# Optimization experiments

Measured on AMD Instinct MI355X. Metric: run time of the kernel, lower is better.

## Reference

```python
import jax, jax.numpy as jnp
import numpy as np

E, D, H, K, T = 16, 1024, 2048, 2, 2048


def setup_inputs() -> dict:
    key = jax.random.key(0)
    k = jax.random.split(key, 7)
    scale = 0.02
    return {
        "inp": jax.random.normal(k[0], (T, D), dtype=jnp.float32),
        "gate_idx": jax.random.randint(k[1], (T, K), 0, E, dtype=jnp.int64),
        "gate_score": jax.random.uniform(k[2], (T, K), dtype=jnp.float32),
        "w1": jax.random.normal(k[3], (E, H, D), dtype=jnp.float32) * scale,
        "b1": jnp.zeros((E, H), dtype=jnp.float32),
        "w2": jax.random.normal(k[4], (E, D, H), dtype=jnp.float32) * scale,
        "b2": jnp.zeros((E, D), dtype=jnp.float32),
    }


def reference(inp, gate_idx, gate_score, w1, b1, w2, b2):
    num_expert = w1.shape[0]
    top_k = gate_idx.shape[1]
    d_model = inp.shape[1]
    # expand each token top_k times (repeat_interleave along dim 0)
    x = jnp.repeat(inp, top_k, axis=0)           # [T*K, D]
    g = gate_idx.reshape(-1)                      # [T*K]
    o = jnp.zeros((x.shape[0], d_model), dtype=x.dtype)
    # static loop over experts; output masked by expert assignment (same math
    # as the per-expert gather/scatter in the original)
    for i in range(num_expert):
        h = jax.nn.gelu(x @ w1[i].T + b1[i])      # [T*K, H]
        y = h @ w2[i].T + b2[i]                   # [T*K, D]
        o = o + jnp.where((g == i)[:, None], y, jnp.zeros((), x.dtype))
    # combine top_k expert outputs with gate scores (bmm in the original)
    out = jnp.einsum("nk,nkd->nd", gate_score, o.reshape(-1, top_k, d_model))
    return out
```

## Files before the change

kernel.cpp:

```cpp
#include <hip/hip_runtime.h>
#include <hip/hip_bf16.h>
#include <stdint.h>


#define E_ 16
#define D_ 1024
#define H_ 2048
#define K_ 2
#define T_ 2048
#define NP_ (T_ * K_)
#define MTS_ 48

using short8 = __attribute__((ext_vector_type(8))) short;
using f32x4  = __attribute__((ext_vector_type(4))) float;

__device__ __forceinline__ unsigned short f2bf(float f) {
  union { float f; unsigned u; } x; x.f = f;
  unsigned r = x.u + 0x7fffu + ((x.u >> 16) & 1u);
  return (unsigned short)(r >> 16);
}

__device__ __forceinline__ float gelu_f(float x) {
  float u = 1.5957691216057308f * (x + 0.044715f * x * x * x);
  return x / (1.f + __expf(-u));
}

__global__ void cvt_kernel(const float* __restrict__ src,
                           unsigned short* __restrict__ dst, int n4) {
  int stride = gridDim.x * blockDim.x;
  for (int i = blockIdx.x * blockDim.x + threadIdx.x; i < n4; i += stride) {
    float4 v = reinterpret_cast<const float4*>(src)[i];
    ushort4 o = make_ushort4(f2bf(v.x), f2bf(v.y), f2bf(v.z), f2bf(v.w));
    reinterpret_cast<ushort4*>(dst)[i] = o;
  }
}

__global__ void route_kernel(const int* __restrict__ gidx,
                             int* __restrict__ rows,
                             int* __restrict__ offsets,
                             int2* __restrict__ tiles) {
  __shared__ int cnt[E_], cur[E_];
  int tid = threadIdx.x;
  if (tid < E_) cnt[tid] = 0;
  __syncthreads();
  for (int p = tid; p < NP_; p += blockDim.x) atomicAdd(&cnt[gidx[p]], 1);
  __syncthreads();
  if (tid == 0) {
    int acc = 0;
    for (int e = 0; e < E_; ++e) { offsets[e] = acc; cur[e] = acc; acc += cnt[e]; }
    offsets[E_] = acc;
    int k = 0;
    for (int e = 0; e < E_; ++e)
      for (int m = offsets[e]; m < offsets[e] + cnt[e]; m += 128)
        tiles[k++] = make_int2(e, m);
    for (; k < MTS_; ++k) tiles[k] = make_int2(-1, 0);
  }
  __syncthreads();
  for (int p = tid; p < NP_; p += blockDim.x) {
    int e = gidx[p];
    int pos = atomicAdd(&cur[e], 1);
    rows[pos] = p;
  }
}

#define GLOAD16(g, l)                                                        \
  __builtin_amdgcn_global_load_lds(                                          \
      (const __attribute__((address_space(1))) unsigned int*)(const void*)(g), \
      (__attribute__((address_space(3))) unsigned int*)(void*)(l), 16, 0, 0)

template<bool IS1>
__global__ __launch_bounds__(256, 3)
void moe_gemm(const unsigned short* __restrict__ A0,
              const float* __restrict__ W,
              const float* __restrict__ bias,
              const int* __restrict__ rows,
              const int* __restrict__ offsets,
              const int2* __restrict__ tiles,
              const float* __restrict__ score,
              unsigned short* __restrict__ Hout,
              float* __restrict__ Yout)
{
  constexpr int BM = 128, BN = 64, BK = 64;
  constexpr int KD = IS1 ? D_ : H_;
  constexpr int NN = IS1 ? H_ : D_;
  constexpr int NT = KD / BK;

  const int2 tile = tiles[blockIdx.y];
  const int e = tile.x;
  if (e < 0) return;
  const int s0   = tile.y;
  const int send = offsets[e + 1];
  const int n0   = blockIdx.x * BN;

  __shared__ unsigned short As[2][BM][BK];
  __shared__ unsigned short Bs[2][BN][BK + 8];
  __shared__ int rowsrc[BM];
  __shared__ int rowdst[BM];

  const int tid  = threadIdx.x;
  const int lane = tid & 63;
  const int wid  = tid >> 6;

  if (tid < BM) {
    int s = s0 + tid;
    bool v = s < send;
    int sc2 = v ? s : s0;
    if (IS1) {
      rowsrc[tid] = rows[sc2] >> 1;
      rowdst[tid] = v ? s : -1;
    } else {
      rowsrc[tid] = sc2;
      rowdst[tid] = v ? rows[s] : -1;
    }
  }
  __syncthreads();

  const int arow  = lane >> 3;
  const int aslot = (lane & 7) ^ arow;
  const unsigned short* gA[4];
#pragma unroll
  for (int i = 0; i < 4; ++i)
    gA[i] = A0 + (size_t)rowsrc[wid * 32 + i * 8 + arow] * KD + aslot * 8;

  const int brow = tid >> 2, bseg = tid & 3;
  const float* gB = W + (size_t)e * NN * KD + (size_t)(n0 + brow) * KD + bseg * 16;

  const int wr = wid >> 1, wc = wid & 1;
  const int fr = lane & 15, fh = lane >> 4;

  f32x4 acc[4][2] = {};
  float4 breg[4];

  auto stageA = [&](int buf, int kk) {
#pragma unroll
    for (int i = 0; i < 4; ++i)
      GLOAD16(gA[i] + kk, &As[buf][wid * 32 + i * 8][0]);
  };
  auto loadB = [&](int kk) {
#pragma unroll
    for (int j = 0; j < 4; ++j)
      breg[j] = *reinterpret_cast<const float4*>(gB + kk + j * 4);
  };
  auto writeB = [&](int buf) {
#pragma unroll
    for (int h = 0; h < 2; ++h) {
      short8 v;
#pragma unroll
      for (int q = 0; q < 4; ++q) v[q]     = (short)f2bf((&breg[2*h].x)[q]);
#pragma unroll
      for (int q = 0; q < 4; ++q) v[4 + q] = (short)f2bf((&breg[2*h+1].x)[q]);
      *reinterpret_cast<short8*>(&Bs[buf][brow][bseg * 16 + h * 8]) = v;
    }
  };
  auto compute = [&](int buf) {
    short8 af[4][2], bv[2][2];
#pragma unroll
    for (int mi = 0; mi < 4; ++mi) {
      const int row = wr * 64 + mi * 16 + fr;
#pragma unroll
      for (int ks = 0; ks < 2; ++ks) {
        const int slot = (ks * 4 + fh) ^ (fr & 7);
        af[mi][ks] = *reinterpret_cast<const short8*>(&As[buf][row][slot * 8]);
      }
    }
#pragma unroll
    for (int ni = 0; ni < 2; ++ni) {
      const int row = wc * 32 + ni * 16 + fr;
#pragma unroll
      for (int ks = 0; ks < 2; ++ks)
        bv[ni][ks] = *reinterpret_cast<const short8*>(&Bs[buf][row][ks * 32 + fh * 8]);
    }
#pragma unroll
    for (int ks = 0; ks < 2; ++ks)
#pragma unroll
      for (int mi = 0; mi < 4; ++mi)
#pragma unroll
        for (int ni = 0; ni < 2; ++ni)
          acc[mi][ni] = __builtin_amdgcn_mfma_f32_16x16x32_bf16(
              af[mi][ks], bv[ni][ks], acc[mi][ni], 0, 0, 0);
  };

  loadB(0);
  stageA(0, 0);
  writeB(0);
  __syncthreads();

  for (int t = 0; t < NT; t += 2) {
    loadB((t + 1) * BK);
    stageA(1, (t + 1) * BK);
    compute(0);
    writeB(1);
    __syncthreads();
    if (t + 2 < NT) { loadB((t + 2) * BK); stageA(0, (t + 2) * BK); }
    compute(1);
    if (t + 2 < NT) writeB(0);
    __syncthreads();
  }

  const float* biasE = bias + (size_t)e * NN + n0;
#pragma unroll
  for (int mi = 0; mi < 4; ++mi) {
#pragma unroll
    for (int j = 0; j < 4; ++j) {
      int rt  = wr * 64 + mi * 16 + fh * 4 + j;
      int dst = rowdst[rt];
      if (dst < 0) continue;
      float sc = IS1 ? 0.f : score[dst];
#pragma unroll
      for (int ni = 0; ni < 2; ++ni) {
        int col = wc * 32 + ni * 16 + fr;
        float v = acc[mi][ni][j] + biasE[col];
        if (IS1) {
          Hout[(size_t)dst * H_ + n0 + col] = f2bf(gelu_f(v));
        } else {
          Yout[(size_t)dst * D_ + n0 + col] = v * sc;
        }
      }
    }
  }
}

__global__ void combine_kernel(const float* __restrict__ y,
                               float* __restrict__ out) {
  const int DQ = D_ / 4;
  int i = blockIdx.x * blockDim.x + threadIdx.x;
  int t = i / DQ, d = i % DQ;
  const float4* y4 = reinterpret_cast<const float4*>(y);
  float4 a = y4[(size_t)(2 * t) * DQ + d];
  float4 b = y4[(size_t)(2 * t + 1) * DQ + d];
  reinterpret_cast<float4*>(out)[i] =
      make_float4(a.x + b.x, a.y + b.y, a.z + b.z, a.w + b.w);
}

extern "C" void kernel_launch(void* const* d_in, const int* in_sizes, int n_in,
                              void* d_out, int out_size, void* d_ws, size_t ws_size,
                              hipStream_t stream) {
  const float* inp    = (const float*)d_in[0];
  const int*   gidx   = (const int*)d_in[1];
  const float* gscore = (const float*)d_in[2];
  const float* w1     = (const float*)d_in[3];
  const float* b1     = (const float*)d_in[4];
  const float* w2     = (const float*)d_in[5];
  const float* b2     = (const float*)d_in[6];
  float* out = (float*)d_out;

  char* ws = (char*)d_ws;
  size_t o = 0;
  auto alloc = [&](size_t bytes) {
    void* p = ws + o;
    o = (o + bytes + 255) & ~(size_t)255;
    return p;
  };
  unsigned short* xb   = (unsigned short*)alloc((size_t)T_ * D_ * 2);
  unsigned short* hbuf = (unsigned short*)alloc((size_t)NP_ * H_ * 2);
  float*          ybuf = (float*)alloc((size_t)NP_ * D_ * 4);
  int*            rows = (int*)alloc(NP_ * 4);
  int*         offsets = (int*)alloc((E_ + 1) * 4);
  int2*          tiles = (int2*)alloc(MTS_ * 8);

  cvt_kernel<<<dim3(256), dim3(256), 0, stream>>>(inp, xb, T_ * D_ / 4);
  route_kernel<<<dim3(1), dim3(256), 0, stream>>>(gidx, rows, offsets, tiles);

  moe_gemm<true><<<dim3(H_ / 64, MTS_, 1), dim3(256), 0, stream>>>(
      xb, w1, b1, rows, offsets, tiles, gscore, hbuf, (float*)nullptr);
  moe_gemm<false><<<dim3(D_ / 64, MTS_, 1), dim3(256), 0, stream>>>(
      hbuf, w2, b2, rows, offsets, tiles, gscore, (unsigned short*)nullptr, ybuf);

  combine_kernel<<<dim3(T_ * D_ / 4 / 256), dim3(256), 0, stream>>>(ybuf, out);
}
```

Before: 171.6 us.

## Deepen GEMM prefetch with two B register sets and explicit vmcnt waits

The MoE GEMM main loop now keeps two tiles of loads in flight, using two register buffers for the fp32 weights and issuing the next A/B loads before converting and storing the current B tile. Raw s_waitcnt and s_barrier with scheduling barriers replace __syncthreads so that outstanding global loads are not fully drained at each barrier. The padded B shared-memory tile is replaced by an XOR-swizzled layout to avoid bank conflicts without padding. The cvt kernel grid is also doubled. The hand-counted vmcnt(8) waits depend on the exact number of loads the compiler emits, so a miscount could let the code read stale LDS.

```diff
diff --git a/kernel.cpp b/kernel.cpp
--- a/kernel.cpp
+++ b/kernel.cpp
@@ -23,6 +23,26 @@
 __device__ __forceinline__ float gelu_f(float x) {
   float u = 1.5957691216057308f * (x + 0.044715f * x * x * x);
   return x / (1.f + __expf(-u));
+}
+
+__device__ __forceinline__ void waitv8() {
+  asm volatile("s_waitcnt vmcnt(8)" ::: "memory");
+  __builtin_amdgcn_sched_barrier(0);
+}
+__device__ __forceinline__ void waitv0() {
+  asm volatile("s_waitcnt vmcnt(0)" ::: "memory");
+  __builtin_amdgcn_sched_barrier(0);
+}
+__device__ __forceinline__ void barrier_only() {
+  __builtin_amdgcn_sched_barrier(0);
+  __builtin_amdgcn_s_barrier();
+  __builtin_amdgcn_sched_barrier(0);
+}
+__device__ __forceinline__ void lgkm0_barrier() {
+  asm volatile("s_waitcnt lgkmcnt(0)" ::: "memory");
+  __builtin_amdgcn_sched_barrier(0);
+  __builtin_amdgcn_s_barrier();
+  __builtin_amdgcn_sched_barrier(0);
 }
 
 __global__ void cvt_kernel(const float* __restrict__ src,
@@ -93,7 +113,7 @@
   const int n0   = blockIdx.x * BN;
 
   __shared__ unsigned short As[2][BM][BK];
-  __shared__ unsigned short Bs[2][BN][BK + 8];
+  __shared__ unsigned short Bs[2][BN][BK];
   __shared__ int rowsrc[BM];
   __shared__ int rowdst[BM];
 
@@ -129,27 +149,28 @@
   const int fr = lane & 15, fh = lane >> 4;
 
   f32x4 acc[4][2] = {};
-  float4 breg[4];
-
-  auto stageA = [&](int buf, int kk) {
+  float4 breg0[4], breg1[4];
+
+  auto issueA = [&](int buf, int kk) {
 #pragma unroll
     for (int i = 0; i < 4; ++i)
       GLOAD16(gA[i] + kk, &As[buf][wid * 32 + i * 8][0]);
   };
-  auto loadB = [&](int kk) {
+  auto issueB = [&](float4* br, int kk) {
 #pragma unroll
     for (int j = 0; j < 4; ++j)
-      breg[j] = *reinterpret_cast<const float4*>(gB + kk + j * 4);
-  };
-  auto writeB = [&](int buf) {
-#pragma unroll
-    for (int h = 0; h < 2; ++h) {
+      br[j] = *reinterpret_cast<const float4*>(gB + kk + j * 4);
+  };
+  auto writeB = [&](int buf, const float4* br) {
+#pragma unroll
+    for (int j = 0; j < 2; ++j) {
       short8 v;
 #pragma unroll
-      for (int q = 0; q < 4; ++q) v[q]     = (short)f2bf((&breg[2*h].x)[q]);
-#pragma unroll
-      for (int q = 0; q < 4; ++q) v[4 + q] = (short)f2bf((&breg[2*h+1].x)[q]);
-      *reinterpret_cast<short8*>(&Bs[buf][brow][bseg * 16 + h * 8]) = v;
+      for (int q = 0; q < 4; ++q) v[q]     = (short)f2bf((&br[2*j].x)[q]);
+#pragma unroll
+      for (int q = 0; q < 4; ++q) v[4 + q] = (short)f2bf((&br[2*j+1].x)[q]);
+      int slot = (bseg * 2 + j) ^ (brow & 7);
+      *reinterpret_cast<short8*>(&Bs[buf][brow][slot * 8]) = v;
     }
   };
   auto compute = [&](int buf) {
@@ -159,7 +180,7 @@
       const int row = wr * 64 + mi * 16 + fr;
 #pragma unroll
       for (int ks = 0; ks < 2; ++ks) {
-        const int slot = (ks * 4 + fh) ^ (fr & 7);
+        const int slot = (ks * 4 + fh) ^ (row & 7);
         af[mi][ks] = *reinterpret_cast<const short8*>(&As[buf][row][slot * 8]);
       }
     }
@@ -167,8 +188,10 @@
     for (int ni = 0; ni < 2; ++ni) {
       const int row = wc * 32 + ni * 16 + fr;
 #pragma unroll
-      for (int ks = 0; ks < 2; ++ks)
-        bv[ni][ks] = *reinterpret_cast<const short8*>(&Bs[buf][row][ks * 32 + fh * 8]);
+      for (int ks = 0; ks < 2; ++ks) {
+        const int slot = (ks * 4 + fh) ^ (row & 7);
+        bv[ni][ks] = *reinterpret_cast<const short8*>(&Bs[buf][row][slot * 8]);
+      }
     }
 #pragma unroll
     for (int ks = 0; ks < 2; ++ks)
@@ -180,21 +203,31 @@
               af[mi][ks], bv[ni][ks], acc[mi][ni], 0, 0, 0);
   };
 
-  loadB(0);
-  stageA(0, 0);
-  writeB(0);
-  __syncthreads();
+  issueA(0, 0);       issueB(breg0, 0);
+  issueA(1, BK);      issueB(breg1, BK);
+  waitv8();
+  writeB(0, breg0);
+  lgkm0_barrier();
 
   for (int t = 0; t < NT; t += 2) {
-    loadB((t + 1) * BK);
-    stageA(1, (t + 1) * BK);
     compute(0);
-    writeB(1);
-    __syncthreads();
-    if (t + 2 < NT) { loadB((t + 2) * BK); stageA(0, (t + 2) * BK); }
+    barrier_only();
+    if (t + 2 < NT) {
+      issueA(0, (t + 2) * BK); issueB(breg0, (t + 2) * BK);
+      waitv8();
+    } else {
+      waitv0();
+    }
+    writeB(1, breg1);
+    lgkm0_barrier();
     compute(1);
-    if (t + 2 < NT) writeB(0);
-    __syncthreads();
+    barrier_only();
+    if (t + 2 < NT) {
+      if (t + 3 < NT) { issueA(1, (t + 3) * BK); issueB(breg1, (t + 3) * BK); waitv8(); }
+      else            { waitv0(); }
+      writeB(0, breg0);
+      lgkm0_barrier();
+    }
   }
 
   const float* biasE = bias + (size_t)e * NN + n0;
@@ -258,7 +291,7 @@
   int*         offsets = (int*)alloc((E_ + 1) * 4);
   int2*          tiles = (int2*)alloc(MTS_ * 8);
 
-  cvt_kernel<<<dim3(256), dim3(256), 0, stream>>>(inp, xb, T_ * D_ / 4);
+  cvt_kernel<<<dim3(512), dim3(256), 0, stream>>>(inp, xb, T_ * D_ / 4);
   route_kernel<<<dim3(1), dim3(256), 0, stream>>>(gidx, rows, offsets, tiles);
 
   moe_gemm<true><<<dim3(H_ / 64, MTS_, 1), dim3(256), 0, stream>>>(
```

Result: faster. 157.1 us (-8.5%).

## Replace LDS-tiled MoE GEMM with register-only flat MFMA kernel

Applied to the files above, without the earlier changes.

Rewrites both expert GEMMs so operands come straight from global memory into registers, with no LDS staging and no barriers. Weights act as the MFMA A operand (128 output features per block) and token rows as B (128 tokens per tile). Loads are double-buffered in registers across K steps of 32. This removes the LDS traffic and syncthreads overhead, at the cost of redundant global/L2 reads of activations per wave, higher register pressure and fewer blocks.

```diff
diff --git a/kernel.cpp b/kernel.cpp
--- a/kernel.cpp
+++ b/kernel.cpp
@@ -63,14 +63,9 @@
   }
 }
 
-#define GLOAD16(g, l)                                                        \
-  __builtin_amdgcn_global_load_lds(                                          \
-      (const __attribute__((address_space(1))) unsigned int*)(const void*)(g), \
-      (__attribute__((address_space(3))) unsigned int*)(void*)(l), 16, 0, 0)
-
 template<bool IS1>
-__global__ __launch_bounds__(256, 3)
-void moe_gemm(const unsigned short* __restrict__ A0,
+__global__ __launch_bounds__(256, 2)
+void moe_flat(const unsigned short* __restrict__ Bsrc,
               const float* __restrict__ W,
               const float* __restrict__ bias,
               const int* __restrict__ rows,
@@ -80,141 +75,101 @@
               unsigned short* __restrict__ Hout,
               float* __restrict__ Yout)
 {
-  constexpr int BM = 128, BN = 64, BK = 64;
   constexpr int KD = IS1 ? D_ : H_;
   constexpr int NN = IS1 ? H_ : D_;
-  constexpr int NT = KD / BK;
+  constexpr int NT = KD / 32;
 
   const int2 tile = tiles[blockIdx.y];
   const int e = tile.x;
   if (e < 0) return;
   const int s0   = tile.y;
   const int send = offsets[e + 1];
-  const int n0   = blockIdx.x * BN;
-
-  __shared__ unsigned short As[2][BM][BK];
-  __shared__ unsigned short Bs[2][BN][BK + 8];
-  __shared__ int rowsrc[BM];
-  __shared__ int rowdst[BM];
-
-  const int tid  = threadIdx.x;
-  const int lane = tid & 63;
-  const int wid  = tid >> 6;
-
-  if (tid < BM) {
-    int s = s0 + tid;
-    bool v = s < send;
-    int sc2 = v ? s : s0;
-    if (IS1) {
-      rowsrc[tid] = rows[sc2] >> 1;
-      rowdst[tid] = v ? s : -1;
-    } else {
-      rowsrc[tid] = sc2;
-      rowdst[tid] = v ? rows[s] : -1;
+
+  const int tid = threadIdx.x, lane = tid & 63, wid = tid >> 6;
+  const int fr = lane & 15, fh = lane >> 4;
+
+  const int abase = blockIdx.x * 128 + wid * 32;
+
+  const float* gA0 = W + ((size_t)e * NN + abase + fr) * KD + fh * 8;
+  const float* gA1 = gA0 + (size_t)16 * KD;
+
+  int boff[8];
+#pragma unroll
+  for (int ni = 0; ni < 8; ++ni) {
+    int slot = s0 + ni * 16 + fr;
+    int cs   = slot < send ? slot : (send - 1);
+    int br   = IS1 ? (rows[cs] >> 1) : cs;
+    boff[ni] = br * KD;
+  }
+  const unsigned short* gBb = Bsrc + fh * 8;
+
+  f32x4 acc[2][8] = {};
+  short8 b0[8], b1[8];
+  float4 a0[2][2], a1[2][2];
+
+  auto loadB = [&](short8* b, int k0) {
+#pragma unroll
+    for (int ni = 0; ni < 8; ++ni)
+      b[ni] = *reinterpret_cast<const short8*>(gBb + boff[ni] + k0);
+  };
+  auto loadA = [&](float4 (*a)[2], int k0) {
+    a[0][0] = *reinterpret_cast<const float4*>(gA0 + k0);
+    a[0][1] = *reinterpret_cast<const float4*>(gA0 + k0 + 4);
+    a[1][0] = *reinterpret_cast<const float4*>(gA1 + k0);
+    a[1][1] = *reinterpret_cast<const float4*>(gA1 + k0 + 4);
+  };
+  auto step = [&](float4 (*a)[2], short8* b) {
+#pragma unroll
+    for (int mi = 0; mi < 2; ++mi) {
+      short8 av;
+      const float* f0 = &a[mi][0].x;
+      const float* f1 = &a[mi][1].x;
+#pragma unroll
+      for (int q = 0; q < 4; ++q) {
+        av[q]     = (short)f2bf(f0[q]);
+        av[4 + q] = (short)f2bf(f1[q]);
+      }
+#pragma unroll
+      for (int ni = 0; ni < 8; ++ni)
+        acc[mi][ni] = __builtin_amdgcn_mfma_f32_16x16x32_bf16(
+            av, b[ni], acc[mi][ni], 0, 0, 0);
     }
-  }
-  __syncthreads();
-
-  const int arow  = lane >> 3;
-  const int aslot = (lane & 7) ^ arow;
-  const unsigned short* gA[4];
-#pragma unroll
-  for (int i = 0; i < 4; ++i)
-    gA[i] = A0 + (size_t)rowsrc[wid * 32 + i * 8 + arow] * KD + aslot * 8;
-
-  const int brow = tid >> 2, bseg = tid & 3;
-  const float* gB = W + (size_t)e * NN * KD + (size_t)(n0 + brow) * KD + bseg * 16;
-
-  const int wr = wid >> 1, wc = wid & 1;
-  const int fr = lane & 15, fh = lane >> 4;
-
-  f32x4 acc[4][2] = {};
-  float4 breg[4];
-
-  auto stageA = [&](int buf, int kk) {
-#pragma unroll
-    for (int i = 0; i < 4; ++i)
-      GLOAD16(gA[i] + kk, &As[buf][wid * 32 + i * 8][0]);
-  };
-  auto loadB = [&](int kk) {
-#pragma unroll
-    for (int j = 0; j < 4; ++j)
-      breg[j] = *reinterpret_cast<const float4*>(gB + kk + j * 4);
-  };
-  auto writeB = [&](int buf) {
-#pragma unroll
-    for (int h = 0; h < 2; ++h) {
-      short8 v;
-#pragma unroll
-      for (int q = 0; q < 4; ++q) v[q]     = (short)f2bf((&breg[2*h].x)[q]);
-#pragma unroll
-      for (int q = 0; q < 4; ++q) v[4 + q] = (short)f2bf((&breg[2*h+1].x)[q]);
-      *reinterpret_cast<short8*>(&Bs[buf][brow][bseg * 16 + h * 8]) = v;
-    }
-  };
-  auto compute = [&](int buf) {
-    short8 af[4][2], bv[2][2];
-#pragma unroll
-    for (int mi = 0; mi < 4; ++mi) {
-      const int row = wr * 64 + mi * 16 + fr;
-#pragma unroll
-      for (int ks = 0; ks < 2; ++ks) {
-        const int slot = (ks * 4 + fh) ^ (fr & 7);
-        af[mi][ks] = *reinterpret_cast<const short8*>(&As[buf][row][slot * 8]);
-      }
-    }
-#pragma unroll
-    for (int ni = 0; ni < 2; ++ni) {
-      const int row = wc * 32 + ni * 16 + fr;
-#pragma unroll
-      for (int ks = 0; ks < 2; ++ks)
-        bv[ni][ks] = *reinterpret_cast<const short8*>(&Bs[buf][row][ks * 32 + fh * 8]);
-    }
-#pragma unroll
-    for (int ks = 0; ks < 2; ++ks)
-#pragma unroll
-      for (int mi = 0; mi < 4; ++mi)
-#pragma unroll
-        for (int ni = 0; ni < 2; ++ni)
-          acc[mi][ni] = __builtin_amdgcn_mfma_f32_16x16x32_bf16(
-              af[mi][ks], bv[ni][ks], acc[mi][ni], 0, 0, 0);
-  };
-
-  loadB(0);
-  stageA(0, 0);
-  writeB(0);
-  __syncthreads();
+  };
+
+  loadB(b0, 0);  loadA(a0, 0);
+  loadB(b1, 32); loadA(a1, 32);
 
   for (int t = 0; t < NT; t += 2) {
-    loadB((t + 1) * BK);
-    stageA(1, (t + 1) * BK);
-    compute(0);
-    writeB(1);
-    __syncthreads();
-    if (t + 2 < NT) { loadB((t + 2) * BK); stageA(0, (t + 2) * BK); }
-    compute(1);
-    if (t + 2 < NT) writeB(0);
-    __syncthreads();
-  }
-
-  const float* biasE = bias + (size_t)e * NN + n0;
-#pragma unroll
-  for (int mi = 0; mi < 4; ++mi) {
-#pragma unroll
-    for (int j = 0; j < 4; ++j) {
-      int rt  = wr * 64 + mi * 16 + fh * 4 + j;
-      int dst = rowdst[rt];
-      if (dst < 0) continue;
-      float sc = IS1 ? 0.f : score[dst];
-#pragma unroll
-      for (int ni = 0; ni < 2; ++ni) {
-        int col = wc * 32 + ni * 16 + fr;
-        float v = acc[mi][ni][j] + biasE[col];
-        if (IS1) {
-          Hout[(size_t)dst * H_ + n0 + col] = f2bf(gelu_f(v));
-        } else {
-          Yout[(size_t)dst * D_ + n0 + col] = v * sc;
-        }
+    step(a0, b0);
+    if (t + 2 < NT) { loadB(b0, (t + 2) * 32); loadA(a0, (t + 2) * 32); }
+    step(a1, b1);
+    if (t + 3 < NT) { loadB(b1, (t + 3) * 32); loadA(a1, (t + 3) * 32); }
+  }
+
+#pragma unroll
+  for (int mi = 0; mi < 2; ++mi) {
+    const int cb = abase + mi * 16 + fh * 4;
+    float4 bs = *reinterpret_cast<const float4*>(bias + (size_t)e * NN + cb);
+#pragma unroll
+    for (int ni = 0; ni < 8; ++ni) {
+      int slot = s0 + ni * 16 + fr;
+      if (slot >= send) continue;
+      if (IS1) {
+        ushort4 hv;
+        hv.x = f2bf(gelu_f(acc[mi][ni][0] + bs.x));
+        hv.y = f2bf(gelu_f(acc[mi][ni][1] + bs.y));
+        hv.z = f2bf(gelu_f(acc[mi][ni][2] + bs.z));
+        hv.w = f2bf(gelu_f(acc[mi][ni][3] + bs.w));
+        *reinterpret_cast<ushort4*>(Hout + (size_t)slot * H_ + cb) = hv;
+      } else {
+        int pair = rows[slot];
+        float sc = score[pair];
+        float4 yv;
+        yv.x = (acc[mi][ni][0] + bs.x) * sc;
+        yv.y = (acc[mi][ni][1] + bs.y) * sc;
+        yv.z = (acc[mi][ni][2] + bs.z) * sc;
+        yv.w = (acc[mi][ni][3] + bs.w) * sc;
+        *reinterpret_cast<float4*>(Yout + (size_t)pair * D_ + cb) = yv;
       }
     }
   }
@@ -258,12 +213,12 @@
   int*         offsets = (int*)alloc((E_ + 1) * 4);
   int2*          tiles = (int2*)alloc(MTS_ * 8);
 
-  cvt_kernel<<<dim3(256), dim3(256), 0, stream>>>(inp, xb, T_ * D_ / 4);
+  cvt_kernel<<<dim3(512), dim3(256), 0, stream>>>(inp, xb, T_ * D_ / 4);
   route_kernel<<<dim3(1), dim3(256), 0, stream>>>(gidx, rows, offsets, tiles);
 
-  moe_gemm<true><<<dim3(H_ / 64, MTS_, 1), dim3(256), 0, stream>>>(
+  moe_flat<true><<<dim3(H_ / 128, MTS_), dim3(256), 0, stream>>>(
       xb, w1, b1, rows, offsets, tiles, gscore, hbuf, (float*)nullptr);
-  moe_gemm<false><<<dim3(D_ / 64, MTS_, 1), dim3(256), 0, stream>>>(
+  moe_flat<false><<<dim3(D_ / 128, MTS_), dim3(256), 0, stream>>>(
       hbuf, w2, b2, rows, offsets, tiles, gscore, (unsigned short*)nullptr, ybuf);
 
   combine_kernel<<<dim3(T_ * D_ / 4 / 256), dim3(256), 0, stream>>>(ybuf, out);
```

Result: slower. 348.0 us (+102.8%).
